# Kernel tuning notes

Hardware: AMD Instinct MI355X
Metric: run time of the kernel (lower is better)

Reference implementation:

```python
import jax, jax.numpy as jnp
import numpy as np

N_GRAPHS = 2048  # number of molecules in the DGL batch


def gcn_layer(h, src, dst, W, residual, n_nodes):
    # DGL sum aggregation: scatter-add neighbor features to dst, then linear + relu
    agg = jax.ops.segment_sum(h[src], dst, num_segments=n_nodes)  # [N, d_in]
    out = jax.nn.relu(agg @ W)  # [N, d_out]
    if residual:
        out = out + h
    return out


def setup_inputs() -> dict:
    key = jax.random.key(0)
    ks = jax.random.split(key, 12)
    N, E, D_N = 100000, 400000, 35
    x = jax.random.normal(ks[0], (N, D_N), dtype=jnp.float32)
    edge_src = jax.random.randint(ks[1], (E,), 0, N)
    edge_dst = jax.random.randint(ks[2], (E,), 0, N)
    graph_ids = jnp.sort(jax.random.randint(ks[3], (N,), 0, N_GRAPHS))
    W_emb = jax.random.normal(ks[4], (D_N, 8), dtype=jnp.float32) * 0.1
    W_g0 = jax.random.normal(ks[5], (8, 128), dtype=jnp.float32) * 0.1
    W_g1 = jax.random.normal(ks[6], (128, 128), dtype=jnp.float32) * 0.05
    W_g2 = jax.random.normal(ks[7], (128, 128), dtype=jnp.float32) * 0.05
    W_p1 = jax.random.normal(ks[8], (128, 64), dtype=jnp.float32) * 0.05
    W_p2 = jax.random.normal(ks[9], (64, 1), dtype=jnp.float32) * 0.05
    b_p2 = jnp.zeros((1,), dtype=jnp.float32)
    return dict(x=x, W_emb=W_emb, W_g0=W_g0, W_g1=W_g1, W_g2=W_g2,
                W_p1=W_p1, W_p2=W_p2, b_p2=b_p2,
                edge_src=edge_src, edge_dst=edge_dst, graph_ids=graph_ids)


def reference(x, W_emb, W_g0, W_g1, W_g2, W_p1, W_p2, b_p2,
              edge_src, edge_dst, graph_ids):
    n = x.shape[0]
    # GCNEmbed: initial node embedding (d_n -> 8, no bias)
    h = x @ W_emb
    # GCN layers: sum aggregation; first layer no residual, rest residual
    h = gcn_layer(h, edge_src, edge_dst, W_g0, False, n)  # 8 -> 128
    h = gcn_layer(h, edge_src, edge_dst, W_g1, True, n)   # 128 -> 128
    h = gcn_layer(h, edge_src, edge_dst, W_g2, True, n)   # 128 -> 128
    # SumPooling over each graph in the batch
    g_emb = jax.ops.segment_sum(h, graph_ids, num_segments=N_GRAPHS)  # [G, 128]
    # pred head: Linear(128,64,no bias) -> ReLU -> Linear(64,1,bias)
    pred = jax.nn.relu(g_emb @ W_p1) @ W_p2 + b_p2  # [G, 1]
    return pred
```

## Files before the change

### kernel.cpp

```cpp
#include <hip/hip_runtime.h>


constexpr int NUM_GRAPHS = 2048;

typedef _Float16 f16x8 __attribute__((ext_vector_type(8)));
typedef float f32x4 __attribute__((ext_vector_type(4)));

__global__ __launch_bounds__(256) void k_embed(const float* __restrict__ x,
                                               const float* __restrict__ Wemb,
                                               float* __restrict__ h0, int N) {
  __shared__ float sx[32 * 35];
  __shared__ float sw[35 * 8];
  int n0 = blockIdx.x * 32;
  int cnt = min(32, N - n0);
  int nf = cnt * 35;
  for (int i = threadIdx.x; i < nf; i += 256) sx[i] = x[(size_t)n0 * 35 + i];
  for (int i = threadIdx.x; i < 35 * 8; i += 256) sw[i] = Wemb[i];
  __syncthreads();
  int nl = threadIdx.x >> 3;
  int c = threadIdx.x & 7;
  if (nl < cnt) {
    float acc = 0.f;
#pragma unroll
    for (int k = 0; k < 35; ++k) acc = fmaf(sx[nl * 35 + k], sw[k * 8 + c], acc);
    h0[(size_t)(n0 + nl) * 8 + c] = acc;
  }
}

__global__ __launch_bounds__(256) void k_hist(const int* __restrict__ dst,
                                              int* counts, int E) {
  int e = blockIdx.x * 256 + threadIdx.x;
  if (e < E) atomicAdd(&counts[dst[e]], 1);
}

__global__ __launch_bounds__(256) void k_scan1(const int* __restrict__ counts,
                                               int* __restrict__ offs,
                                               int* __restrict__ partials, int N) {
  __shared__ int s[256];
  int i = blockIdx.x * 256 + threadIdx.x;
  int v = (i < N) ? counts[i] : 0;
  s[threadIdx.x] = v;
  __syncthreads();
#pragma unroll
  for (int d = 1; d < 256; d <<= 1) {
    int t = (threadIdx.x >= d) ? s[threadIdx.x - d] : 0;
    __syncthreads();
    s[threadIdx.x] += t;
    __syncthreads();
  }
  if (i < N) offs[i] = s[threadIdx.x] - v;
  if (threadIdx.x == 255) partials[blockIdx.x] = s[255];
}

__global__ __launch_bounds__(512) void k_scan2(int* partials, int nb) {
  __shared__ int s[512];
  int t = threadIdx.x;
  int orig = (t < nb) ? partials[t] : 0;
  s[t] = orig;
  __syncthreads();
#pragma unroll
  for (int d = 1; d < 512; d <<= 1) {
    int v = (t >= d) ? s[t - d] : 0;
    __syncthreads();
    s[t] += v;
    __syncthreads();
  }
  if (t < nb) partials[t] = s[t] - orig;
}

__global__ __launch_bounds__(256) void k_scan3(int* __restrict__ offs,
                                               const int* __restrict__ partials,
                                               int* __restrict__ cursor, int N) {
  int i = blockIdx.x * 256 + threadIdx.x;
  if (i < N) {
    int v = offs[i] + partials[blockIdx.x];
    offs[i] = v;
    cursor[i] = v;
  }
}

__global__ __launch_bounds__(256) void k_fill(const int* __restrict__ src,
                                              const int* __restrict__ dst,
                                              int* cursor, int* __restrict__ csr,
                                              int E) {
  int e = blockIdx.x * 256 + threadIdx.x;
  if (e < E) {
    int slot = atomicAdd(&cursor[dst[e]], 1);
    csr[slot] = src[e];
  }
}

__global__ __launch_bounds__(128) void k_prepw(const float* __restrict__ W1,
                                               const float* __restrict__ W2,
                                               _Float16* __restrict__ WT1,
                                               _Float16* __restrict__ WT2) {
  int n = blockIdx.x & 127;
  const float* W = (blockIdx.x < 128) ? W1 : W2;
  _Float16* WT = (blockIdx.x < 128) ? WT1 : WT2;
  int k = threadIdx.x;
  WT[(size_t)n * 128 + k] = (_Float16)W[(size_t)k * 128 + n];
}

__global__ __launch_bounds__(256) void k_layer0(const float* __restrict__ h0,
                                                const int* __restrict__ csr,
                                                const int* __restrict__ offs,
                                                const int* __restrict__ cnts,
                                                const float* __restrict__ W,
                                                _Float16* __restrict__ out, int N) {
  __shared__ float sagg[32 * 9];
  __shared__ float sw[8 * 128];
  for (int i = threadIdx.x; i < 1024; i += 256) sw[i] = W[i];
  int n0 = blockIdx.x * 32;
  {
    int i = threadIdx.x >> 3;
    int c = threadIdx.x & 7;
    int n = n0 + i;
    float acc = 0.f;
    if (n < N) {
      int s = offs[n], cc = cnts[n];
      for (int e = 0; e < cc; ++e) acc += h0[(size_t)csr[s + e] * 8 + c];
    }
    sagg[i * 9 + c] = acc;
  }
  __syncthreads();
  int i2 = threadIdx.x >> 3;
  int j0 = (threadIdx.x & 7) * 16;
  int n2 = n0 + i2;
  if (n2 >= N) return;
  float a[8];
#pragma unroll
  for (int k = 0; k < 8; ++k) a[k] = sagg[i2 * 9 + k];
  float og[16];
#pragma unroll
  for (int j = 0; j < 16; ++j) og[j] = 0.f;
#pragma unroll
  for (int k = 0; k < 8; ++k)
#pragma unroll
    for (int j = 0; j < 16; ++j) og[j] = fmaf(a[k], sw[k * 128 + j0 + j], og[j]);
  size_t base = (size_t)n2 * 128 + j0;
  f16x8 o0, o1;
#pragma unroll
  for (int j = 0; j < 8; ++j) {
    o0[j] = (_Float16)fmaxf(og[j], 0.f);
    o1[j] = (_Float16)fmaxf(og[8 + j], 0.f);
  }
  *reinterpret_cast<f16x8*>(out + base) = o0;
  *reinterpret_cast<f16x8*>(out + base + 8) = o1;
}

__device__ __forceinline__ void acc_f16x8(float4& a0, float4& a1, const f16x8 h) {
  a0.x += (float)h[0]; a0.y += (float)h[1]; a0.z += (float)h[2]; a0.w += (float)h[3];
  a1.x += (float)h[4]; a1.y += (float)h[5]; a1.z += (float)h[6]; a1.w += (float)h[7];
}

__global__ __launch_bounds__(256, 4) void k_gcn_fused(
    const _Float16* __restrict__ H, const int* __restrict__ csr,
    const int* __restrict__ offs, const int* __restrict__ cnts,
    const _Float16* __restrict__ WT, _Float16* __restrict__ out,
    float* G, const int* __restrict__ gid, int N, int E, int mode) {
  __shared__ _Float16 sa_h[64 * 136];
  int* sidx = reinterpret_cast<int*>(sa_h);
  int n0 = blockIdx.x * 64;

  int e0 = offs[n0];
  int e1 = (n0 + 64 < N) ? offs[n0 + 64] : E;
  int nedge = e1 - e0;
  bool staged = (nedge <= 64 * 136 / 2);

  if (staged) {
    for (int i = threadIdx.x; i < nedge; i += 256) sidx[i] = csr[e0 + i];
  }
  __syncthreads();

  int q = threadIdx.x >> 6;
  int l = threadIdx.x & 63;
  {
    int n = n0 + l;
    float4 acc[8];
#pragma unroll
    for (int i = 0; i < 8; ++i) acc[i] = make_float4(0.f, 0.f, 0.f, 0.f);
    int cnt = (n < N) ? cnts[n] : 0;
    int sb = (n < N) ? (offs[n] - e0) : 0;
    const _Float16* Hq = H + q * 32;
    if (staged) {
      int e = 0;
      for (; e + 4 <= cnt; e += 4) {
        int s0 = sidx[sb + e], s1 = sidx[sb + e + 1];
        int s2 = sidx[sb + e + 2], s3 = sidx[sb + e + 3];
        const f16x8* r0 = reinterpret_cast<const f16x8*>(Hq + (size_t)s0 * 128);
        const f16x8* r1 = reinterpret_cast<const f16x8*>(Hq + (size_t)s1 * 128);
        const f16x8* r2 = reinterpret_cast<const f16x8*>(Hq + (size_t)s2 * 128);
        const f16x8* r3 = reinterpret_cast<const f16x8*>(Hq + (size_t)s3 * 128);
        f16x8 a0 = r0[0], a1 = r0[1], a2 = r0[2], a3 = r0[3];
        f16x8 b0 = r1[0], b1 = r1[1], b2 = r1[2], b3 = r1[3];
        f16x8 c0 = r2[0], c1 = r2[1], c2 = r2[2], c3 = r2[3];
        f16x8 d0 = r3[0], d1 = r3[1], d2 = r3[2], d3 = r3[3];
        acc_f16x8(acc[0], acc[1], a0); acc_f16x8(acc[2], acc[3], a1);
        acc_f16x8(acc[4], acc[5], a2); acc_f16x8(acc[6], acc[7], a3);
        acc_f16x8(acc[0], acc[1], b0); acc_f16x8(acc[2], acc[3], b1);
        acc_f16x8(acc[4], acc[5], b2); acc_f16x8(acc[6], acc[7], b3);
        acc_f16x8(acc[0], acc[1], c0); acc_f16x8(acc[2], acc[3], c1);
        acc_f16x8(acc[4], acc[5], c2); acc_f16x8(acc[6], acc[7], c3);
        acc_f16x8(acc[0], acc[1], d0); acc_f16x8(acc[2], acc[3], d1);
        acc_f16x8(acc[4], acc[5], d2); acc_f16x8(acc[6], acc[7], d3);
      }
      for (; e < cnt; ++e) {
        int s0 = sidx[sb + e];
        const f16x8* r0 = reinterpret_cast<const f16x8*>(Hq + (size_t)s0 * 128);
        f16x8 a0 = r0[0], a1 = r0[1], a2 = r0[2], a3 = r0[3];
        acc_f16x8(acc[0], acc[1], a0); acc_f16x8(acc[2], acc[3], a1);
        acc_f16x8(acc[4], acc[5], a2); acc_f16x8(acc[6], acc[7], a3);
      }
    } else {
      int s = (n < N) ? offs[n] : 0;
      for (int e = 0; e < cnt; ++e) {
        int s0 = csr[s + e];
        const f16x8* r0 = reinterpret_cast<const f16x8*>(Hq + (size_t)s0 * 128);
        f16x8 a0 = r0[0], a1 = r0[1], a2 = r0[2], a3 = r0[3];
        acc_f16x8(acc[0], acc[1], a0); acc_f16x8(acc[2], acc[3], a1);
        acc_f16x8(acc[4], acc[5], a2); acc_f16x8(acc[6], acc[7], a3);
      }
    }
    __syncthreads();
    float* af = reinterpret_cast<float*>(acc);
#pragma unroll
    for (int j = 0; j < 4; ++j) {
      f16x8 st;
#pragma unroll
      for (int i = 0; i < 8; ++i) st[i] = (_Float16)af[j * 8 + i];
      *reinterpret_cast<f16x8*>(&sa_h[l * 136 + q * 32 + j * 8]) = st;
    }
  }
  __syncthreads();

  {
    int w = threadIdx.x >> 6;
    int lane = threadIdx.x & 63;
    int lr = lane & 15;
    int lg = lane >> 4;
    f32x4 C[4][2];
#pragma unroll
    for (int mt = 0; mt < 4; ++mt)
#pragma unroll
      for (int nt = 0; nt < 2; ++nt) C[mt][nt] = (f32x4){0.f, 0.f, 0.f, 0.f};
    const _Float16* WTb = WT + (size_t)(w * 32) * 128;
#pragma unroll
    for (int kk = 0; kk < 4; ++kk) {
      int k0 = kk * 32 + lg * 8;
      f16x8 a0 = *reinterpret_cast<const f16x8*>(&sa_h[(0 + lr) * 136 + k0]);
      f16x8 a1 = *reinterpret_cast<const f16x8*>(&sa_h[(16 + lr) * 136 + k0]);
      f16x8 a2 = *reinterpret_cast<const f16x8*>(&sa_h[(32 + lr) * 136 + k0]);
      f16x8 a3 = *reinterpret_cast<const f16x8*>(&sa_h[(48 + lr) * 136 + k0]);
      f16x8 b0 = *reinterpret_cast<const f16x8*>(&WTb[(size_t)lr * 128 + k0]);
      f16x8 b1 = *reinterpret_cast<const f16x8*>(&WTb[(size_t)(16 + lr) * 128 + k0]);
      C[0][0] = __builtin_amdgcn_mfma_f32_16x16x32_f16(a0, b0, C[0][0], 0, 0, 0);
      C[1][0] = __builtin_amdgcn_mfma_f32_16x16x32_f16(a1, b0, C[1][0], 0, 0, 0);
      C[2][0] = __builtin_amdgcn_mfma_f32_16x16x32_f16(a2, b0, C[2][0], 0, 0, 0);
      C[3][0] = __builtin_amdgcn_mfma_f32_16x16x32_f16(a3, b0, C[3][0], 0, 0, 0);
      C[0][1] = __builtin_amdgcn_mfma_f32_16x16x32_f16(a0, b1, C[0][1], 0, 0, 0);
      C[1][1] = __builtin_amdgcn_mfma_f32_16x16x32_f16(a1, b1, C[1][1], 0, 0, 0);
      C[2][1] = __builtin_amdgcn_mfma_f32_16x16x32_f16(a2, b1, C[2][1], 0, 0, 0);
      C[3][1] = __builtin_amdgcn_mfma_f32_16x16x32_f16(a3, b1, C[3][1], 0, 0, 0);
    }
    __syncthreads();
#pragma unroll
    for (int mt = 0; mt < 4; ++mt)
#pragma unroll
      for (int nt = 0; nt < 2; ++nt)
#pragma unroll
        for (int r = 0; r < 4; ++r) {
          int row = mt * 16 + lg * 4 + r;
          int col = w * 32 + nt * 16 + lr;
          sa_h[row * 136 + col] = (_Float16)fmaxf(C[mt][nt][r], 0.f);
        }
  }
  __syncthreads();

  int nl = threadIdx.x >> 4;
  int j0 = (threadIdx.x & 15) * 8;
  if (mode == 0) {
#pragma unroll
    for (int r = 0; r < 4; ++r) {
      int row = nl + 16 * r;
      int n = n0 + row;
      if (n < N) {
        size_t base = (size_t)n * 128 + j0;
        f16x8 vv = *reinterpret_cast<const f16x8*>(&sa_h[row * 136 + j0]);
        f16x8 hh = *reinterpret_cast<const f16x8*>(H + base);
        f16x8 o;
#pragma unroll
        for (int i = 0; i < 8; ++i) o[i] = (_Float16)((float)vv[i] + (float)hh[i]);
        *reinterpret_cast<f16x8*>(out + base) = o;
      }
    }
  } else {
#pragma unroll
    for (int r = 0; r < 4; ++r) {
      int row = nl + 16 * r;
      int n = n0 + row;
      if (n < N) {
        size_t base = (size_t)n * 128 + j0;
        f16x8 vv = *reinterpret_cast<const f16x8*>(&sa_h[row * 136 + j0]);
        f16x8 hh = *reinterpret_cast<const f16x8*>(H + base);
        f16x8 o;
#pragma unroll
        for (int i = 0; i < 8; ++i) o[i] = (_Float16)((float)vv[i] + (float)hh[i]);
        *reinterpret_cast<f16x8*>(&sa_h[row * 136 + j0]) = o;
      }
    }
    __syncthreads();
    int grp = threadIdx.x >> 7;
    int j = threadIdx.x & 127;
    int r0 = grp * 32;
    int nfirst = n0 + r0;
    if (nfirst < N) {
      float pacc = 0.f;
      int cur = gid[nfirst];
      for (int r = r0; r < r0 + 32; ++r) {
        int n = n0 + r;
        if (n >= N) break;
        int g2 = gid[n];
        if (g2 != cur) {
          atomicAdd(&G[(size_t)cur * 128 + j], pacc);
          pacc = 0.f;
          cur = g2;
        }
        pacc += (float)sa_h[r * 136 + j];
      }
      atomicAdd(&G[(size_t)cur * 128 + j], pacc);
    }
  }
}

__global__ __launch_bounds__(64) void k_head(const float* __restrict__ g,
                                             const float* __restrict__ W1,
                                             const float* __restrict__ W2,
                                             const float* __restrict__ b,
                                             float* __restrict__ out) {
  int gi = blockIdx.x;
  int j = threadIdx.x;
  __shared__ float sg[128];
  sg[j] = g[(size_t)gi * 128 + j];
  sg[j + 64] = g[(size_t)gi * 128 + 64 + j];
  __syncthreads();
  float acc = 0.f;
#pragma unroll
  for (int k = 0; k < 128; ++k) acc = fmaf(sg[k], W1[k * 64 + j], acc);
  acc = fmaxf(acc, 0.f) * W2[j];
#pragma unroll
  for (int off = 32; off > 0; off >>= 1) acc += __shfl_down(acc, off);
  if (j == 0) out[gi] = acc + b[0];
}

extern "C" void kernel_launch(void* const* d_in, const int* in_sizes, int n_in,
                              void* d_out, int out_size, void* d_ws, size_t ws_size,
                              hipStream_t stream) {
  const float* x    = (const float*)d_in[0];
  const float* Wemb = (const float*)d_in[1];
  const float* Wg0  = (const float*)d_in[2];
  const float* Wg1  = (const float*)d_in[3];
  const float* Wg2  = (const float*)d_in[4];
  const float* Wp1  = (const float*)d_in[5];
  const float* Wp2  = (const float*)d_in[6];
  const float* bp2  = (const float*)d_in[7];
  const int* esrc   = (const int*)d_in[8];
  const int* edst   = (const int*)d_in[9];
  const int* gids   = (const int*)d_in[10];
  int N = in_sizes[0] / 35;
  int E = in_sizes[8];
  float* out = (float*)d_out;

  char* wp = (char*)d_ws;
  float* h0 = (float*)wp;            wp += (size_t)N * 8 * sizeof(float);
  _Float16* P = (_Float16*)wp;       wp += (size_t)N * 128 * sizeof(_Float16);
  _Float16* Q = (_Float16*)wp;       wp += (size_t)N * 128 * sizeof(_Float16);
  float* G  = (float*)wp;            wp += (size_t)NUM_GRAPHS * 128 * sizeof(float);
  int* counts   = (int*)wp;          wp += (size_t)N * sizeof(int);
  int* offs     = (int*)wp;          wp += (size_t)N * sizeof(int);
  int* cursor   = (int*)wp;          wp += (size_t)N * sizeof(int);
  int* partials = (int*)wp;          wp += 512 * sizeof(int);
  int* csr      = (int*)wp;          wp += (size_t)E * sizeof(int);
  _Float16* WT1 = (_Float16*)wp;     wp += (size_t)128 * 128 * sizeof(_Float16);
  _Float16* WT2 = (_Float16*)wp;

  int nbE = (E + 255) / 256;
  int nbN = (N + 255) / 256;

  k_embed<<<(N + 31) / 32, 256, 0, stream>>>(x, Wemb, h0, N);
  k_prepw<<<256, 128, 0, stream>>>(Wg1, Wg2, WT1, WT2);

  hipMemsetAsync(counts, 0, (size_t)N * sizeof(int), stream);
  k_hist<<<nbE, 256, 0, stream>>>(edst, counts, E);
  k_scan1<<<nbN, 256, 0, stream>>>(counts, offs, partials, N);
  k_scan2<<<1, 512, 0, stream>>>(partials, nbN);
  k_scan3<<<nbN, 256, 0, stream>>>(offs, partials, cursor, N);
  k_fill<<<nbE, 256, 0, stream>>>(esrc, edst, cursor, csr, E);

  hipMemsetAsync(G, 0, (size_t)NUM_GRAPHS * 128 * sizeof(float), stream);

  k_layer0<<<(N + 31) / 32, 256, 0, stream>>>(h0, csr, offs, counts, Wg0, P, N);

  k_gcn_fused<<<(N + 63) / 64, 256, 0, stream>>>(P, csr, offs, counts, WT1, Q,
                                                 nullptr, nullptr, N, E, 0);

  k_gcn_fused<<<(N + 63) / 64, 256, 0, stream>>>(Q, csr, offs, counts, WT2, nullptr,
                                                 G, gids, N, E, 1);

  k_head<<<NUM_GRAPHS, 64, 0, stream>>>(G, Wp1, Wp2, bp2, out);
}
```

Measured before the change: 166.8 us.

## Restructure layer0 to one node per thread with staged CSR and masked 4-way gathers

Layer0 is rewritten so each thread owns one node and gathers all 8 features with float4 loads, using CSR indices staged in shared memory, then computes the 8x128 projection itself. The edge loops in layer0 and the fused GCN kernel now always process four neighbors per iteration. Out-of-range neighbors are clamped to a valid index and masked with a zero scale in an FMA, which removes the scalar tail loop. A sched_barrier keeps all gather loads issued ahead of the accumulations so more memory requests are in flight. The cost is redundant loads for padded edges, higher per-thread register use in layer0, and fewer, larger blocks.

```diff
diff --git a/kernel.cpp b/kernel.cpp
--- a/kernel.cpp
+++ b/kernel.cpp
@@ -101,56 +101,108 @@
   WT[(size_t)n * 128 + k] = (_Float16)W[(size_t)k * 128 + n];
 }
 
-__global__ __launch_bounds__(256) void k_layer0(const float* __restrict__ h0,
-                                                const int* __restrict__ csr,
-                                                const int* __restrict__ offs,
-                                                const int* __restrict__ cnts,
-                                                const float* __restrict__ W,
-                                                _Float16* __restrict__ out, int N) {
-  __shared__ float sagg[32 * 9];
+__global__ __launch_bounds__(256, 4) void k_layer0(const float* __restrict__ h0,
+                                                   const int* __restrict__ csr,
+                                                   const int* __restrict__ offs,
+                                                   const int* __restrict__ cnts,
+                                                   const float* __restrict__ W,
+                                                   _Float16* __restrict__ out,
+                                                   int N, int E) {
+  __shared__ int sidx0[6144];
   __shared__ float sw[8 * 128];
   for (int i = threadIdx.x; i < 1024; i += 256) sw[i] = W[i];
-  int n0 = blockIdx.x * 32;
-  {
-    int i = threadIdx.x >> 3;
-    int c = threadIdx.x & 7;
-    int n = n0 + i;
-    float acc = 0.f;
-    if (n < N) {
-      int s = offs[n], cc = cnts[n];
-      for (int e = 0; e < cc; ++e) acc += h0[(size_t)csr[s + e] * 8 + c];
-    }
-    sagg[i * 9 + c] = acc;
-  }
-  __syncthreads();
-  int i2 = threadIdx.x >> 3;
-  int j0 = (threadIdx.x & 7) * 16;
-  int n2 = n0 + i2;
-  if (n2 >= N) return;
-  float a[8];
-#pragma unroll
-  for (int k = 0; k < 8; ++k) a[k] = sagg[i2 * 9 + k];
-  float og[16];
-#pragma unroll
-  for (int j = 0; j < 16; ++j) og[j] = 0.f;
-#pragma unroll
-  for (int k = 0; k < 8; ++k)
-#pragma unroll
-    for (int j = 0; j < 16; ++j) og[j] = fmaf(a[k], sw[k * 128 + j0 + j], og[j]);
-  size_t base = (size_t)n2 * 128 + j0;
-  f16x8 o0, o1;
-#pragma unroll
-  for (int j = 0; j < 8; ++j) {
-    o0[j] = (_Float16)fmaxf(og[j], 0.f);
-    o1[j] = (_Float16)fmaxf(og[8 + j], 0.f);
-  }
-  *reinterpret_cast<f16x8*>(out + base) = o0;
-  *reinterpret_cast<f16x8*>(out + base + 8) = o1;
+  int n0 = blockIdx.x * 256;
+  int e0 = offs[n0];
+  int e1 = (n0 + 256 < N) ? offs[n0 + 256] : E;
+  int nedge = e1 - e0;
+  bool staged = (nedge <= 6144);
+  if (staged) {
+    for (int i = threadIdx.x; i < nedge; i += 256) sidx0[i] = csr[e0 + i];
+  }
+  __syncthreads();
+
+  int n = n0 + (int)threadIdx.x;
+  float4 A0 = {0.f, 0.f, 0.f, 0.f}, A1 = {0.f, 0.f, 0.f, 0.f};
+  int cnt = (n < N) ? cnts[n] : 0;
+  int sb = (n < N) ? (offs[n] - e0) : 0;
+  if (staged) {
+    for (int e = 0; e < cnt; e += 4) {
+      int i0 = sidx0[sb + e];
+      int i1 = sidx0[sb + min(e + 1, cnt - 1)];
+      int i2 = sidx0[sb + min(e + 2, cnt - 1)];
+      int i3 = sidx0[sb + min(e + 3, cnt - 1)];
+      float s1 = (e + 1 < cnt) ? 1.f : 0.f;
+      float s2 = (e + 2 < cnt) ? 1.f : 0.f;
+      float s3 = (e + 3 < cnt) ? 1.f : 0.f;
+      const float4* p0 = reinterpret_cast<const float4*>(h0 + (size_t)i0 * 8);
+      const float4* p1 = reinterpret_cast<const float4*>(h0 + (size_t)i1 * 8);
+      const float4* p2 = reinterpret_cast<const float4*>(h0 + (size_t)i2 * 8);
+      const float4* p3 = reinterpret_cast<const float4*>(h0 + (size_t)i3 * 8);
+      float4 a0 = p0[0], a1 = p0[1];
+      float4 b0 = p1[0], b1 = p1[1];
+      float4 c0 = p2[0], c1 = p2[1];
+      float4 d0 = p3[0], d1 = p3[1];
+      __builtin_amdgcn_sched_barrier(0);
+      A0.x += a0.x; A0.y += a0.y; A0.z += a0.z; A0.w += a0.w;
+      A1.x += a1.x; A1.y += a1.y; A1.z += a1.z; A1.w += a1.w;
+      A0.x = fmaf(s1, b0.x, A0.x); A0.y = fmaf(s1, b0.y, A0.y);
+      A0.z = fmaf(s1, b0.z, A0.z); A0.w = fmaf(s1, b0.w, A0.w);
+      A1.x = fmaf(s1, b1.x, A1.x); A1.y = fmaf(s1, b1.y, A1.y);
+      A1.z = fmaf(s1, b1.z, A1.z); A1.w = fmaf(s1, b1.w, A1.w);
+      A0.x = fmaf(s2, c0.x, A0.x); A0.y = fmaf(s2, c0.y, A0.y);
+      A0.z = fmaf(s2, c0.z, A0.z); A0.w = fmaf(s2, c0.w, A0.w);
+      A1.x = fmaf(s2, c1.x, A1.x); A1.y = fmaf(s2, c1.y, A1.y);
+      A1.z = fmaf(s2, c1.z, A1.z); A1.w = fmaf(s2, c1.w, A1.w);
+      A0.x = fmaf(s3, d0.x, A0.x); A0.y = fmaf(s3, d0.y, A0.y);
+      A0.z = fmaf(s3, d0.z, A0.z); A0.w = fmaf(s3, d0.w, A0.w);
+      A1.x = fmaf(s3, d1.x, A1.x); A1.y = fmaf(s3, d1.y, A1.y);
+      A1.z = fmaf(s3, d1.z, A1.z); A1.w = fmaf(s3, d1.w, A1.w);
+    }
+  } else {
+    for (int e = 0; e < cnt; ++e) {
+      int i0 = csr[offs[n] + e];
+      const float4* p0 = reinterpret_cast<const float4*>(h0 + (size_t)i0 * 8);
+      float4 a0 = p0[0], a1 = p0[1];
+      A0.x += a0.x; A0.y += a0.y; A0.z += a0.z; A0.w += a0.w;
+      A1.x += a1.x; A1.y += a1.y; A1.z += a1.z; A1.w += a1.w;
+    }
+  }
+  if (n >= N) return;
+
+  float a[8] = {A0.x, A0.y, A0.z, A0.w, A1.x, A1.y, A1.z, A1.w};
+  size_t base = (size_t)n * 128;
+#pragma unroll
+  for (int c0 = 0; c0 < 128; c0 += 32) {
+    float o[32];
+#pragma unroll
+    for (int j = 0; j < 32; ++j) o[j] = 0.f;
+#pragma unroll
+    for (int k = 0; k < 8; ++k) {
+      float av = a[k];
+      const float* swk = &sw[k * 128 + c0];
+#pragma unroll
+      for (int j = 0; j < 32; ++j) o[j] = fmaf(av, swk[j], o[j]);
+    }
+#pragma unroll
+    for (int v = 0; v < 4; ++v) {
+      f16x8 st;
+#pragma unroll
+      for (int i = 0; i < 8; ++i) st[i] = (_Float16)fmaxf(o[v * 8 + i], 0.f);
+      *reinterpret_cast<f16x8*>(out + base + c0 + v * 8) = st;
+    }
+  }
 }
 
 __device__ __forceinline__ void acc_f16x8(float4& a0, float4& a1, const f16x8 h) {
   a0.x += (float)h[0]; a0.y += (float)h[1]; a0.z += (float)h[2]; a0.w += (float)h[3];
   a1.x += (float)h[4]; a1.y += (float)h[5]; a1.z += (float)h[6]; a1.w += (float)h[7];
+}
+__device__ __forceinline__ void acc_fma8(float4& a0, float4& a1, const f16x8 h,
+                                         float s) {
+  a0.x = fmaf(s, (float)h[0], a0.x); a0.y = fmaf(s, (float)h[1], a0.y);
+  a0.z = fmaf(s, (float)h[2], a0.z); a0.w = fmaf(s, (float)h[3], a0.w);
+  a1.x = fmaf(s, (float)h[4], a1.x); a1.y = fmaf(s, (float)h[5], a1.y);
+  a1.z = fmaf(s, (float)h[6], a1.z); a1.w = fmaf(s, (float)h[7], a1.w);
 }
 
 __global__ __launch_bounds__(256, 4) void k_gcn_fused(
@@ -183,33 +235,31 @@
     int sb = (n < N) ? (offs[n] - e0) : 0;
     const _Float16* Hq = H + q * 32;
     if (staged) {
-      int e = 0;
-      for (; e + 4 <= cnt; e += 4) {
-        int s0 = sidx[sb + e], s1 = sidx[sb + e + 1];
-        int s2 = sidx[sb + e + 2], s3 = sidx[sb + e + 3];
-        const f16x8* r0 = reinterpret_cast<const f16x8*>(Hq + (size_t)s0 * 128);
-        const f16x8* r1 = reinterpret_cast<const f16x8*>(Hq + (size_t)s1 * 128);
-        const f16x8* r2 = reinterpret_cast<const f16x8*>(Hq + (size_t)s2 * 128);
-        const f16x8* r3 = reinterpret_cast<const f16x8*>(Hq + (size_t)s3 * 128);
+      for (int e = 0; e < cnt; e += 4) {
+        int i0 = sidx[sb + e];
+        int i1 = sidx[sb + min(e + 1, cnt - 1)];
+        int i2 = sidx[sb + min(e + 2, cnt - 1)];
+        int i3 = sidx[sb + min(e + 3, cnt - 1)];
+        float s1 = (e + 1 < cnt) ? 1.f : 0.f;
+        float s2 = (e + 2 < cnt) ? 1.f : 0.f;
+        float s3 = (e + 3 < cnt) ? 1.f : 0.f;
+        const f16x8* r0 = reinterpret_cast<const f16x8*>(Hq + (size_t)i0 * 128);
+        const f16x8* r1 = reinterpret_cast<const f16x8*>(Hq + (size_t)i1 * 128);
+        const f16x8* r2 = reinterpret_cast<const f16x8*>(Hq + (size_t)i2 * 128);
+        const f16x8* r3 = reinterpret_cast<const f16x8*>(Hq + (size_t)i3 * 128);
         f16x8 a0 = r0[0], a1 = r0[1], a2 = r0[2], a3 = r0[3];
         f16x8 b0 = r1[0], b1 = r1[1], b2 = r1[2], b3 = r1[3];
         f16x8 c0 = r2[0], c1 = r2[1], c2 = r2[2], c3 = r2[3];
         f16x8 d0 = r3[0], d1 = r3[1], d2 = r3[2], d3 = r3[3];
+        __builtin_amdgcn_sched_barrier(0);
         acc_f16x8(acc[0], acc[1], a0); acc_f16x8(acc[2], acc[3], a1);
         acc_f16x8(acc[4], acc[5], a2); acc_f16x8(acc[6], acc[7], a3);
-        acc_f16x8(acc[0], acc[1], b0); acc_f16x8(acc[2], acc[3], b1);
-        acc_f16x8(acc[4], acc[5], b2); acc_f16x8(acc[6], acc[7], b3);
-        acc_f16x8(acc[0], acc[1], c0); acc_f16x8(acc[2], acc[3], c1);
-        acc_f16x8(acc[4], acc[5], c2); acc_f16x8(acc[6], acc[7], c3);
-        acc_f16x8(acc[0], acc[1], d0); acc_f16x8(acc[2], acc[3], d1);
-        acc_f16x8(acc[4], acc[5], d2); acc_f16x8(acc[6], acc[7], d3);
-      }
-      for (; e < cnt; ++e) {
-        int s0 = sidx[sb + e];
-        const f16x8* r0 = reinterpret_cast<const f16x8*>(Hq + (size_t)s0 * 128);
-        f16x8 a0 = r0[0], a1 = r0[1], a2 = r0[2], a3 = r0[3];
-        acc_f16x8(acc[0], acc[1], a0); acc_f16x8(acc[2], acc[3], a1);
-        acc_f16x8(acc[4], acc[5], a2); acc_f16x8(acc[6], acc[7], a3);
+        acc_fma8(acc[0], acc[1], b0, s1); acc_fma8(acc[2], acc[3], b1, s1);
+        acc_fma8(acc[4], acc[5], b2, s1); acc_fma8(acc[6], acc[7], b3, s1);
+        acc_fma8(acc[0], acc[1], c0, s2); acc_fma8(acc[2], acc[3], c1, s2);
+        acc_fma8(acc[4], acc[5], c2, s2); acc_fma8(acc[6], acc[7], c3, s2);
+        acc_fma8(acc[0], acc[1], d0, s3); acc_fma8(acc[2], acc[3], d1, s3);
+        acc_fma8(acc[4], acc[5], d2, s3); acc_fma8(acc[6], acc[7], d3, s3);
       }
     } else {
       int s = (n < N) ? offs[n] : 0;
@@ -398,7 +448,8 @@
 
   hipMemsetAsync(G, 0, (size_t)NUM_GRAPHS * 128 * sizeof(float), stream);
 
-  k_layer0<<<(N + 31) / 32, 256, 0, stream>>>(h0, csr, offs, counts, Wg0, P, N);
+  k_layer0<<<(N + 255) / 256, 256, 0, stream>>>(h0, csr, offs, counts, Wg0, P,
+                                                N, E);
 
   k_gcn_fused<<<(N + 63) / 64, 256, 0, stream>>>(P, csr, offs, counts, WT1, Q,
                                                  nullptr, nullptr, N, E, 0);
```

Result: slower. 172.7 us (+3.5%).

## Double-buffer neighbor gathers in fused GCN aggregation and branchless remainder

Applied to the files above, without the earlier changes.

Software-pipelines the staged edge-gather loop with two register buffers of 16 f16x8 loads, issuing the next group of four neighbor-row loads before accumulating the current group, so memory latency overlaps with the adds. The 1-3 edge remainder is now handled in one step with masked FMAs, reusing the last index for padding instead of a serial per-edge loop. Launch bounds drop from 4 to 2 blocks per SM to give room for the larger register footprint, which lowers the occupancy available for hiding latency.

```diff
diff --git a/kernel.cpp b/kernel.cpp
--- a/kernel.cpp
+++ b/kernel.cpp
@@ -152,8 +152,42 @@
   a0.x += (float)h[0]; a0.y += (float)h[1]; a0.z += (float)h[2]; a0.w += (float)h[3];
   a1.x += (float)h[4]; a1.y += (float)h[5]; a1.z += (float)h[6]; a1.w += (float)h[7];
 }
-
-__global__ __launch_bounds__(256, 4) void k_gcn_fused(
+__device__ __forceinline__ void acc_fma8(float4& a0, float4& a1, const f16x8 h,
+                                         float s) {
+  a0.x = fmaf(s, (float)h[0], a0.x); a0.y = fmaf(s, (float)h[1], a0.y);
+  a0.z = fmaf(s, (float)h[2], a0.z); a0.w = fmaf(s, (float)h[3], a0.w);
+  a1.x = fmaf(s, (float)h[4], a1.x); a1.y = fmaf(s, (float)h[5], a1.y);
+  a1.z = fmaf(s, (float)h[6], a1.z); a1.w = fmaf(s, (float)h[7], a1.w);
+}
+
+#define LOADG(BUF, G)                                                         \
+  {                                                                           \
+    int b_ = sb + ((G) << 2);                                                 \
+    int i0_ = sidx[b_], i1_ = sidx[b_ + 1];                                   \
+    int i2_ = sidx[b_ + 2], i3_ = sidx[b_ + 3];                               \
+    const f16x8* r0_ = reinterpret_cast<const f16x8*>(Hq + (size_t)i0_ * 128);\
+    const f16x8* r1_ = reinterpret_cast<const f16x8*>(Hq + (size_t)i1_ * 128);\
+    const f16x8* r2_ = reinterpret_cast<const f16x8*>(Hq + (size_t)i2_ * 128);\
+    const f16x8* r3_ = reinterpret_cast<const f16x8*>(Hq + (size_t)i3_ * 128);\
+    BUF[0] = r0_[0]; BUF[1] = r0_[1]; BUF[2] = r0_[2]; BUF[3] = r0_[3];       \
+    BUF[4] = r1_[0]; BUF[5] = r1_[1]; BUF[6] = r1_[2]; BUF[7] = r1_[3];       \
+    BUF[8] = r2_[0]; BUF[9] = r2_[1]; BUF[10] = r2_[2]; BUF[11] = r2_[3];     \
+    BUF[12] = r3_[0]; BUF[13] = r3_[1]; BUF[14] = r3_[2]; BUF[15] = r3_[3];   \
+  }
+
+#define MATHG(BUF)                                                            \
+  {                                                                           \
+    acc_f16x8(acc[0], acc[1], BUF[0]); acc_f16x8(acc[2], acc[3], BUF[1]);     \
+    acc_f16x8(acc[4], acc[5], BUF[2]); acc_f16x8(acc[6], acc[7], BUF[3]);     \
+    acc_f16x8(acc[0], acc[1], BUF[4]); acc_f16x8(acc[2], acc[3], BUF[5]);     \
+    acc_f16x8(acc[4], acc[5], BUF[6]); acc_f16x8(acc[6], acc[7], BUF[7]);     \
+    acc_f16x8(acc[0], acc[1], BUF[8]); acc_f16x8(acc[2], acc[3], BUF[9]);     \
+    acc_f16x8(acc[4], acc[5], BUF[10]); acc_f16x8(acc[6], acc[7], BUF[11]);   \
+    acc_f16x8(acc[0], acc[1], BUF[12]); acc_f16x8(acc[2], acc[3], BUF[13]);   \
+    acc_f16x8(acc[4], acc[5], BUF[14]); acc_f16x8(acc[6], acc[7], BUF[15]);   \
+  }
+
+__global__ __launch_bounds__(256, 2) void k_gcn_fused(
     const _Float16* __restrict__ H, const int* __restrict__ csr,
     const int* __restrict__ offs, const int* __restrict__ cnts,
     const _Float16* __restrict__ WT, _Float16* __restrict__ out,
@@ -183,33 +217,40 @@
     int sb = (n < N) ? (offs[n] - e0) : 0;
     const _Float16* Hq = H + q * 32;
     if (staged) {
-      int e = 0;
-      for (; e + 4 <= cnt; e += 4) {
-        int s0 = sidx[sb + e], s1 = sidx[sb + e + 1];
-        int s2 = sidx[sb + e + 2], s3 = sidx[sb + e + 3];
-        const f16x8* r0 = reinterpret_cast<const f16x8*>(Hq + (size_t)s0 * 128);
-        const f16x8* r1 = reinterpret_cast<const f16x8*>(Hq + (size_t)s1 * 128);
-        const f16x8* r2 = reinterpret_cast<const f16x8*>(Hq + (size_t)s2 * 128);
-        const f16x8* r3 = reinterpret_cast<const f16x8*>(Hq + (size_t)s3 * 128);
-        f16x8 a0 = r0[0], a1 = r0[1], a2 = r0[2], a3 = r0[3];
-        f16x8 b0 = r1[0], b1 = r1[1], b2 = r1[2], b3 = r1[3];
-        f16x8 c0 = r2[0], c1 = r2[1], c2 = r2[2], c3 = r2[3];
-        f16x8 d0 = r3[0], d1 = r3[1], d2 = r3[2], d3 = r3[3];
-        acc_f16x8(acc[0], acc[1], a0); acc_f16x8(acc[2], acc[3], a1);
-        acc_f16x8(acc[4], acc[5], a2); acc_f16x8(acc[6], acc[7], a3);
-        acc_f16x8(acc[0], acc[1], b0); acc_f16x8(acc[2], acc[3], b1);
-        acc_f16x8(acc[4], acc[5], b2); acc_f16x8(acc[6], acc[7], b3);
-        acc_f16x8(acc[0], acc[1], c0); acc_f16x8(acc[2], acc[3], c1);
-        acc_f16x8(acc[4], acc[5], c2); acc_f16x8(acc[6], acc[7], c3);
-        acc_f16x8(acc[0], acc[1], d0); acc_f16x8(acc[2], acc[3], d1);
-        acc_f16x8(acc[4], acc[5], d2); acc_f16x8(acc[6], acc[7], d3);
-      }
-      for (; e < cnt; ++e) {
-        int s0 = sidx[sb + e];
-        const f16x8* r0 = reinterpret_cast<const f16x8*>(Hq + (size_t)s0 * 128);
-        f16x8 a0 = r0[0], a1 = r0[1], a2 = r0[2], a3 = r0[3];
-        acc_f16x8(acc[0], acc[1], a0); acc_f16x8(acc[2], acc[3], a1);
-        acc_f16x8(acc[4], acc[5], a2); acc_f16x8(acc[6], acc[7], a3);
+      int ngf = cnt >> 2;
+      int rem = cnt & 3;
+      f16x8 Abuf[16], Bbuf[16];
+      if (ngf > 0) {
+        LOADG(Abuf, 0);
+        int g = 0;
+        for (; g + 1 < ngf; g += 2) {
+          LOADG(Bbuf, g + 1);
+          MATHG(Abuf);
+          if (g + 2 < ngf) LOADG(Abuf, g + 2);
+          MATHG(Bbuf);
+        }
+        if (g < ngf) MATHG(Abuf);
+      }
+      if (rem) {
+        int b_ = sb + (ngf << 2);
+        int lastv = sidx[sb + cnt - 1];
+        int i0 = sidx[b_];
+        int i1 = (rem > 1) ? sidx[b_ + 1] : lastv;
+        int i2 = (rem > 2) ? sidx[b_ + 2] : lastv;
+        float s1 = (rem > 1) ? 1.f : 0.f;
+        float s2 = (rem > 2) ? 1.f : 0.f;
+        const f16x8* r0 = reinterpret_cast<const f16x8*>(Hq + (size_t)i0 * 128);
+        const f16x8* r1 = reinterpret_cast<const f16x8*>(Hq + (size_t)i1 * 128);
+        const f16x8* r2 = reinterpret_cast<const f16x8*>(Hq + (size_t)i2 * 128);
+        f16x8 t0 = r0[0], t1 = r0[1], t2 = r0[2], t3 = r0[3];
+        f16x8 u0 = r1[0], u1 = r1[1], u2 = r1[2], u3 = r1[3];
+        f16x8 v0 = r2[0], v1 = r2[1], v2 = r2[2], v3 = r2[3];
+        acc_f16x8(acc[0], acc[1], t0); acc_f16x8(acc[2], acc[3], t1);
+        acc_f16x8(acc[4], acc[5], t2); acc_f16x8(acc[6], acc[7], t3);
+        acc_fma8(acc[0], acc[1], u0, s1); acc_fma8(acc[2], acc[3], u1, s1);
+        acc_fma8(acc[4], acc[5], u2, s1); acc_fma8(acc[6], acc[7], u3, s1);
+        acc_fma8(acc[0], acc[1], v0, s2); acc_fma8(acc[2], acc[3], v1, s2);
+        acc_fma8(acc[4], acc[5], v2, s2); acc_fma8(acc[6], acc[7], v3, s2);
       }
     } else {
       int s = (n < N) ? offs[n] : 0;
```

Result: slower. 192.5 us (+15.4%).
